# Kernel tuning notes

Hardware: AMD Instinct MI355X
Metric: run time of the kernel (lower is better)

## Reference

```python
import jax, jax.numpy as jnp
import numpy as np

B, S, D, H = 1, 256, 128, 4
HD = D // H          # 32
EPS = 1e-5
SCALE = 1.0 / float(np.sqrt(HD))


def setup_inputs() -> dict:
    key = jax.random.key(0)
    ks = jax.random.split(key, 6)
    pair = jax.random.normal(ks[0], (B, S, S, D), dtype=jnp.float32)
    ln_w = jnp.ones((D,), dtype=jnp.float32)
    wq = jax.random.normal(ks[1], (D, D), dtype=jnp.float32) * 0.05
    wk = jax.random.normal(ks[2], (D, D), dtype=jnp.float32) * 0.05
    wv = jax.random.normal(ks[3], (D, D), dtype=jnp.float32) * 0.05
    wo = jax.random.normal(ks[4], (D, D), dtype=jnp.float32) * 0.05
    return {"pair": pair, "ln_w": ln_w, "wq": wq, "wk": wk, "wv": wv, "wo": wo}


def reference(pair, ln_w, wq, wk, wv, wo):
    b, s, _, d = pair.shape
    h, hd = H, HD
    # LayerNorm (weight only, no bias) over last dim
    mu = jnp.mean(pair, axis=-1, keepdims=True)
    var = jnp.mean((pair - mu) ** 2, axis=-1, keepdims=True)
    xn = (pair - mu) * jax.lax.rsqrt(var + EPS) * ln_w
    # starting=True: no transpose of the pair axes
    q = (xn @ wq.T).reshape(b, s, s, h, hd)
    k = (xn @ wk.T).reshape(b, s, s, h, hd)
    v = (xn @ wv.T).reshape(b, s, s, h, hd)
    # attention over the second seq axis (j), independent per row i
    scores = jnp.einsum("biqhd,bikhd->bihqk", q, k) * SCALE  # [b,i,h,q,k]
    p = jax.nn.softmax(scores, axis=-1)
    out = jnp.einsum("bihqk,bikhd->biqhd", p, v).reshape(b, s, s, d)
    return out @ wo.T
```

## Files before the change

kernel.cpp:

```cpp
#include <hip/hip_runtime.h>
#include <hip/hip_bf16.h>
#include <math.h>

#define S 256
#define D 128
#define H 4
#define HD 32
#define NT (S * S)

constexpr float EPS = 1e-5f;
constexpr float EXPC = 0.17677669529663687f * 1.44269504088896f;

typedef short bf16x8 __attribute__((ext_vector_type(8)));
typedef float floatx4 __attribute__((ext_vector_type(4)));

union BfBits { __hip_bfloat16 b; unsigned short u; };
__device__ inline unsigned short f2bf_bits(float f) {
  BfBits t;
  t.b = __float2bfloat16(f);
  return t.u;
}
__device__ inline short f2bf_s(float f) { return (short)f2bf_bits(f); }
__device__ inline float bfbits2f(unsigned short u) {
  union { float f; unsigned int i; } t;
  t.i = ((unsigned int)u) << 16;
  return t.f;
}
__device__ inline void split_bf(float x, unsigned short& hi, unsigned short& lo) {
  hi = f2bf_bits(x);
  lo = f2bf_bits(x - bfbits2f(hi));
}
__device__ inline unsigned int pk2(float a, float b) {
  return (unsigned int)f2bf_bits(a) | ((unsigned int)f2bf_bits(b) << 16);
}

__global__ __launch_bounds__(256) void wsplit_kernel(
    const float* __restrict__ wq, const float* __restrict__ wk,
    const float* __restrict__ wv, const float* __restrict__ wo,
    unsigned short* __restrict__ whi, unsigned short* __restrict__ wlo) {
  int idx = blockIdx.x * 256 + threadIdx.x;
  const float* srcs[4] = {wq, wk, wv, wo};
#pragma unroll
  for (int m = 0; m < 4; m++) {
    unsigned short hi, lo;
    split_bf(srcs[m][idx], hi, lo);
    whi[m * 16384 + idx] = hi;
    wlo[m * 16384 + idx] = lo;
  }
}

#define XS(row, col) ((col) ^ (((row) & 7) << 3))

__global__ __launch_bounds__(512, 2) void fused_tri_kernel(
    const float* __restrict__ pair, const float* __restrict__ ln_w,
    const unsigned short* __restrict__ Whi,
    const unsigned short* __restrict__ Wlo, float* __restrict__ out) {
  __shared__ unsigned short xn[256][D];
  __shared__ unsigned int kvpool[8192];
  unsigned short* Kt = (unsigned short*)kvpool;
  unsigned short* Vt = (unsigned short*)kvpool + 8192;
  unsigned int* Ost = kvpool;

  const int i = blockIdx.x;
  const int w = (int)(threadIdx.x >> 6);
  const int lane = (int)(threadIdx.x & 63);
  const int c16 = lane & 15;
  const int quad = lane >> 4;
  const int h = w >> 1;
  const int half = w & 1;

  {
    float4 w0 = *(const float4*)(ln_w + c16 * 8);
    float4 w1 = *(const float4*)(ln_w + c16 * 8 + 4);
#pragma unroll
    for (int g = 0; g < 8; g++) {
      const int tok = w * 32 + g * 4 + quad;
      const float* src = pair + ((size_t)i * S + tok) * D + c16 * 8;
      float4 x0 = *(const float4*)(src);
      float4 x1 = *(const float4*)(src + 4);
      float s = (x0.x + x0.y) + (x0.z + x0.w) + (x1.x + x1.y) + (x1.z + x1.w);
      s += __shfl_xor(s, 1);
      s += __shfl_xor(s, 2);
      s += __shfl_xor(s, 4);
      s += __shfl_xor(s, 8);
      const float mu = s * (1.0f / D);
      float a[8];
      a[0] = x0.x - mu; a[1] = x0.y - mu; a[2] = x0.z - mu; a[3] = x0.w - mu;
      a[4] = x1.x - mu; a[5] = x1.y - mu; a[6] = x1.z - mu; a[7] = x1.w - mu;
      float vs = 0.f;
#pragma unroll
      for (int r = 0; r < 8; r++) vs = fmaf(a[r], a[r], vs);
      vs += __shfl_xor(vs, 1);
      vs += __shfl_xor(vs, 2);
      vs += __shfl_xor(vs, 4);
      vs += __shfl_xor(vs, 8);
      const float rinv = rsqrtf(vs * (1.0f / D) + EPS);
      const float wv8[8] = {w0.x, w0.y, w0.z, w0.w, w1.x, w1.y, w1.z, w1.w};
      unsigned int u[4];
#pragma unroll
      for (int r = 0; r < 4; r++) {
        unsigned int h0 = f2bf_bits(a[2 * r] * rinv * wv8[2 * r]);
        unsigned int h1 = f2bf_bits(a[2 * r + 1] * rinv * wv8[2 * r + 1]);
        u[r] = h0 | (h1 << 16);
      }
      uint4 st = {u[0], u[1], u[2], u[3]};
      *(uint4*)&xn[tok][XS(tok, c16 * 8)] = st;
    }
  }
  __syncthreads();

  bf16x8 qf[8];
  {
#pragma unroll
    for (int r = 0; r < 2; r++) {
      floatx4 acc[2][4];
#pragma unroll
      for (int mi = 0; mi < 2; mi++)
#pragma unroll
        for (int nt = 0; nt < 4; nt++) acc[mi][nt] = (floatx4){0.f, 0.f, 0.f, 0.f};
#pragma unroll
      for (int ks = 0; ks < 4; ks++) {
        bf16x8 bh[4];
#pragma unroll
        for (int nt = 0; nt < 4; nt++) {
          const int row = half * 128 + r * 64 + nt * 16 + c16;
          bh[nt] = *(const bf16x8*)&xn[row][XS(row, ks * 32 + quad * 8)];
        }
#pragma unroll
        for (int mi = 0; mi < 2; mi++) {
          const int arow = h * 32 + mi * 16 + c16;
          bf16x8 ah = *(const bf16x8*)(Whi + arow * D + ks * 32 + quad * 8);
          bf16x8 al = *(const bf16x8*)(Wlo + arow * D + ks * 32 + quad * 8);
#pragma unroll
          for (int nt = 0; nt < 4; nt++) {
            acc[mi][nt] = __builtin_amdgcn_mfma_f32_16x16x32_bf16(ah, bh[nt], acc[mi][nt], 0, 0, 0);
            acc[mi][nt] = __builtin_amdgcn_mfma_f32_16x16x32_bf16(al, bh[nt], acc[mi][nt], 0, 0, 0);
          }
        }
      }
      const int srcL = c16 + (quad & 1) * 32;
      const int srcH = srcL + 16;
      const bool hi2 = quad >= 2;
#pragma unroll
      for (int nt = 0; nt < 4; nt++) {
        int pa = (int)pk2(acc[0][nt][0], acc[0][nt][1]);
        int pb = (int)pk2(acc[0][nt][2], acc[0][nt][3]);
        int pc = (int)pk2(acc[1][nt][0], acc[1][nt][1]);
        int pd = (int)pk2(acc[1][nt][2], acc[1][nt][3]);
        int aL = __shfl(pa, srcL), cL = __shfl(pc, srcL);
        int bL = __shfl(pb, srcL), dL = __shfl(pd, srcL);
        int aH = __shfl(pa, srcH), cH = __shfl(pc, srcH);
        int bH = __shfl(pb, srcH), dH = __shfl(pd, srcH);
        union { unsigned int u[4]; bf16x8 v; } qq;
        qq.u[0] = (unsigned int)(hi2 ? cL : aL);
        qq.u[1] = (unsigned int)(hi2 ? dL : bL);
        qq.u[2] = (unsigned int)(hi2 ? cH : aH);
        qq.u[3] = (unsigned int)(hi2 ? dH : bH);
        qf[r * 4 + nt] = qq.v;
      }
    }
  }

  floatx4 att[2][8];
#pragma unroll
  for (int dt = 0; dt < 2; dt++)
#pragma unroll
    for (int qt = 0; qt < 8; qt++) att[dt][qt] = (floatx4){0.f, 0.f, 0.f, 0.f};
  float lsum[8] = {0.f, 0.f, 0.f, 0.f, 0.f, 0.f, 0.f, 0.f};
  const int permc = ((c16 >> 2) * 8) + (c16 & 3);

  for (int jt = 0; jt < 4; jt++) {
    __syncthreads();
    {
      const int hb = half * 16;
      const unsigned short* wkh = Whi + 16384;
      const unsigned short* wkl = Wlo + 16384;
      const unsigned short* wvh = Whi + 32768;
      const unsigned short* wvl = Wlo + 32768;
      floatx4 ak[4], av[4];
#pragma unroll
      for (int nt = 0; nt < 4; nt++) {
        ak[nt] = (floatx4){0.f, 0.f, 0.f, 0.f};
        av[nt] = (floatx4){0.f, 0.f, 0.f, 0.f};
      }
#pragma unroll
      for (int ks = 0; ks < 4; ks++) {
        bf16x8 bh[4];
#pragma unroll
        for (int nt = 0; nt < 4; nt++) {
          const int row = jt * 64 + nt * 16 + c16;
          bh[nt] = *(const bf16x8*)&xn[row][XS(row, ks * 32 + quad * 8)];
        }
        const int arow = h * 32 + hb + c16;
        bf16x8 kh = *(const bf16x8*)(wkh + arow * D + ks * 32 + quad * 8);
        bf16x8 kl = *(const bf16x8*)(wkl + arow * D + ks * 32 + quad * 8);
        bf16x8 vh = *(const bf16x8*)(wvh + arow * D + ks * 32 + quad * 8);
        bf16x8 vl = *(const bf16x8*)(wvl + arow * D + ks * 32 + quad * 8);
#pragma unroll
        for (int nt = 0; nt < 4; nt++) {
          ak[nt] = __builtin_amdgcn_mfma_f32_16x16x32_bf16(kh, bh[nt], ak[nt], 0, 0, 0);
          ak[nt] = __builtin_amdgcn_mfma_f32_16x16x32_bf16(kl, bh[nt], ak[nt], 0, 0, 0);
          av[nt] = __builtin_amdgcn_mfma_f32_16x16x32_bf16(vh, bh[nt], av[nt], 0, 0, 0);
          av[nt] = __builtin_amdgcn_mfma_f32_16x16x32_bf16(vl, bh[nt], av[nt], 0, 0, 0);
        }
      }
      const int c2 = half * 2 + (quad >> 1);
#pragma unroll
      for (int nt = 0; nt < 4; nt++) {
        const int jl = nt * 16 + c16;
        ushort4 pkk;
        pkk.x = f2bf_bits(ak[nt][0]);
        pkk.y = f2bf_bits(ak[nt][1]);
        pkk.z = f2bf_bits(ak[nt][2]);
        pkk.w = f2bf_bits(ak[nt][3]);
        *(ushort4*)(Kt + h * 2048 + c2 * 512 + jl * 8 + (quad & 1) * 4) = pkk;
#pragma unroll
        for (int r2 = 0; r2 < 4; r2++) {
          const int hd = hb + quad * 4 + r2;
          Vt[h * 2048 + hd * 64 + (((jl >> 3) ^ (hd & 7)) << 3) + (jl & 7)] =
              f2bf_bits(av[nt][r2]);
        }
      }
    }
    __syncthreads();
#pragma unroll
    for (int jb = 0; jb < 2; jb++) {
      const int jbl = jb * 32;
      bf16x8 kf0 = *(const bf16x8*)(Kt + h * 2048 + quad * 512 + (jbl + permc) * 8);
      bf16x8 kf1 = *(const bf16x8*)(Kt + h * 2048 + quad * 512 + (jbl + permc + 4) * 8);
      const int ch = (jbl >> 3) + quad;
      bf16x8 vf0 = *(const bf16x8*)(Vt + h * 2048 + c16 * 64 + ((ch ^ (c16 & 7)) << 3));
      bf16x8 vf1 = *(const bf16x8*)(Vt + h * 2048 + (16 + c16) * 64 + ((ch ^ (c16 & 7)) << 3));
#pragma unroll
      for (int qt = 0; qt < 8; qt++) {
        floatx4 s0 = __builtin_amdgcn_mfma_f32_16x16x32_bf16(
            kf0, qf[qt], (floatx4){0.f, 0.f, 0.f, 0.f}, 0, 0, 0);
        floatx4 s1 = __builtin_amdgcn_mfma_f32_16x16x32_bf16(
            kf1, qf[qt], (floatx4){0.f, 0.f, 0.f, 0.f}, 0, 0, 0);
        float pr[8];
#pragma unroll
        for (int r = 0; r < 4; r++) pr[r] = exp2f(s0[r] * EXPC);
#pragma unroll
        for (int r = 0; r < 4; r++) pr[4 + r] = exp2f(s1[r] * EXPC);
        float ls = 0.f;
#pragma unroll
        for (int r = 0; r < 8; r++) ls += pr[r];
        lsum[qt] += ls;
        bf16x8 pf;
#pragma unroll
        for (int r = 0; r < 8; r++) pf[r] = f2bf_s(pr[r]);
        att[0][qt] = __builtin_amdgcn_mfma_f32_16x16x32_bf16(vf0, pf, att[0][qt], 0, 0, 0);
        att[1][qt] = __builtin_amdgcn_mfma_f32_16x16x32_bf16(vf1, pf, att[1][qt], 0, 0, 0);
      }
    }
  }

#pragma unroll
  for (int qt = 0; qt < 8; qt++) {
    float l = lsum[qt];
    l += __shfl_xor(l, 16);
    l += __shfl_xor(l, 32);
    lsum[qt] = 1.0f / l;
  }

  bf16x8 woh[4], wol[4];
#pragma unroll
  for (int ks = 0; ks < 4; ks++) {
    woh[ks] = *(const bf16x8*)(Whi + 3 * 16384 + (w * 16 + c16) * D + ks * 32 + quad * 8);
    wol[ks] = *(const bf16x8*)(Wlo + 3 * 16384 + (w * 16 + c16) * D + ks * 32 + quad * 8);
  }

#pragma unroll
  for (int cc = 0; cc < 4; cc++) {
    __syncthreads();
    if ((cc >> 1) == half) {
#pragma unroll
      for (int t = 0; t < 4; t++) {
        const int qg = (cc & 1) * 4 + t;
        const float inv = lsum[qg];
        const int tok = t * 16 + c16;
#pragma unroll
        for (int dt = 0; dt < 2; dt++) {
          floatx4 v4 = att[dt][qg];
          unsigned int u[4];
          unsigned short hh, ll;
          split_bf(v4[0] * inv, hh, ll); u[0] = (unsigned)hh | ((unsigned)ll << 16);
          split_bf(v4[1] * inv, hh, ll); u[1] = (unsigned)hh | ((unsigned)ll << 16);
          split_bf(v4[2] * inv, hh, ll); u[2] = (unsigned)hh | ((unsigned)ll << 16);
          split_bf(v4[3] * inv, hh, ll); u[3] = (unsigned)hh | ((unsigned)ll << 16);
          const int chunk = h * 8 + dt * 4 + quad;
          uint4 st = {u[0], u[1], u[2], u[3]};
          *(uint4*)(Ost + tok * 128 + ((chunk ^ c16) << 2)) = st;
        }
      }
    }
    __syncthreads();
    floatx4 oacc[4];
#pragma unroll
    for (int nt = 0; nt < 4; nt++) oacc[nt] = (floatx4){0.f, 0.f, 0.f, 0.f};
#pragma unroll
    for (int ks = 0; ks < 4; ks++) {
#pragma unroll
      for (int nt = 0; nt < 4; nt++) {
        const int tok = nt * 16 + c16;
        const int ch0 = ks * 8 + quad * 2;
        uint4 u0 = *(const uint4*)(Ost + tok * 128 + ((ch0 ^ c16) << 2));
        uint4 u1 = *(const uint4*)(Ost + tok * 128 + (((ch0 + 1) ^ c16) << 2));
        unsigned int bhw[4], blw[4];
        bhw[0] = (u0.x & 0xFFFFu) | (u0.y << 16);
        blw[0] = (u0.x >> 16) | (u0.y & 0xFFFF0000u);
        bhw[1] = (u0.z & 0xFFFFu) | (u0.w << 16);
        blw[1] = (u0.z >> 16) | (u0.w & 0xFFFF0000u);
        bhw[2] = (u1.x & 0xFFFFu) | (u1.y << 16);
        blw[2] = (u1.x >> 16) | (u1.y & 0xFFFF0000u);
        bhw[3] = (u1.z & 0xFFFFu) | (u1.w << 16);
        blw[3] = (u1.z >> 16) | (u1.w & 0xFFFF0000u);
        bf16x8 bh = *(bf16x8*)bhw;
        bf16x8 bl = *(bf16x8*)blw;
        oacc[nt] = __builtin_amdgcn_mfma_f32_16x16x32_bf16(woh[ks], bh, oacc[nt], 0, 0, 0);
        oacc[nt] = __builtin_amdgcn_mfma_f32_16x16x32_bf16(woh[ks], bl, oacc[nt], 0, 0, 0);
        oacc[nt] = __builtin_amdgcn_mfma_f32_16x16x32_bf16(wol[ks], bh, oacc[nt], 0, 0, 0);
      }
    }
#pragma unroll
    for (int nt = 0; nt < 4; nt++) {
      float4 st4;
      st4.x = oacc[nt][0];
      st4.y = oacc[nt][1];
      st4.z = oacc[nt][2];
      st4.w = oacc[nt][3];
      *(float4*)(out + ((size_t)i * S + cc * 64 + nt * 16 + c16) * D + w * 16 + quad * 4) = st4;
    }
  }
}

extern "C" void kernel_launch(void* const* d_in, const int* in_sizes, int n_in,
                              void* d_out, int out_size, void* d_ws,
                              size_t ws_size, hipStream_t stream) {
  const float* pair = (const float*)d_in[0];
  const float* ln_w = (const float*)d_in[1];
  const float* wq = (const float*)d_in[2];
  const float* wk = (const float*)d_in[3];
  const float* wv = (const float*)d_in[4];
  const float* wo = (const float*)d_in[5];
  float* out = (float*)d_out;

  unsigned short* Whi = (unsigned short*)d_ws;
  unsigned short* Wlo = Whi + 4 * 16384;

  wsplit_kernel<<<64, 256, 0, stream>>>(wq, wk, wv, wo, Whi, Wlo);
  fused_tri_kernel<<<S, 512, 0, stream>>>(pair, ln_w, Whi, Wlo, out);
}
```

Before: 159.5 us.

## Double-buffer K/V tiles to overlap projection with attention, plus load batching

K/V projection for the next 64-token tile is now computed into registers while attention consumes the current tile from a second shared-memory buffer, which removes one barrier per iteration and lets MFMA projection overlap softmax work. Several smaller changes come with it. All pair loads are issued before the LayerNorm math, and the Q weight fragments are hoisted out of the k-loop. The softmax scale is folded into Q before packing to bf16. The output projection is retiled 32x32 per wave and drops the first barrier. The cost is double the shared memory for K/V and more live registers, which could hurt occupancy under launch_bounds(512,2), and prescaling Q changes bf16 rounding slightly.

```diff
diff --git a/kernel.cpp b/kernel.cpp
--- a/kernel.cpp
+++ b/kernel.cpp
@@ -51,15 +51,111 @@
 
 #define XS(row, col) ((col) ^ (((row) & 7) << 3))
 
+__device__ __forceinline__ floatx4 MF(bf16x8 a, bf16x8 b, floatx4 c) {
+  return __builtin_amdgcn_mfma_f32_16x16x32_bf16(a, b, c, 0, 0, 0);
+}
+
+__device__ __forceinline__ void kv_mfma(const unsigned short (*xn)[D],
+                                        const unsigned short* __restrict__ Whi,
+                                        const unsigned short* __restrict__ Wlo,
+                                        int jt, int h, int hb, int c16,
+                                        int quad, floatx4 ak[4], floatx4 av[4]) {
+  const unsigned short* wkh = Whi + 16384;
+  const unsigned short* wkl = Wlo + 16384;
+  const unsigned short* wvh = Whi + 32768;
+  const unsigned short* wvl = Wlo + 32768;
+  const int arow = h * 32 + hb + c16;
+#pragma unroll
+  for (int nt = 0; nt < 4; nt++) {
+    ak[nt] = (floatx4){0.f, 0.f, 0.f, 0.f};
+    av[nt] = (floatx4){0.f, 0.f, 0.f, 0.f};
+  }
+#pragma unroll
+  for (int ks = 0; ks < 4; ks++) {
+    bf16x8 bh[4];
+#pragma unroll
+    for (int nt = 0; nt < 4; nt++) {
+      const int row = jt * 64 + nt * 16 + c16;
+      bh[nt] = *(const bf16x8*)&xn[row][XS(row, ks * 32 + quad * 8)];
+    }
+    bf16x8 kh = *(const bf16x8*)(wkh + arow * D + ks * 32 + quad * 8);
+    bf16x8 kl = *(const bf16x8*)(wkl + arow * D + ks * 32 + quad * 8);
+    bf16x8 vh = *(const bf16x8*)(wvh + arow * D + ks * 32 + quad * 8);
+    bf16x8 vl = *(const bf16x8*)(wvl + arow * D + ks * 32 + quad * 8);
+#pragma unroll
+    for (int nt = 0; nt < 4; nt++) {
+      ak[nt] = MF(kh, bh[nt], ak[nt]);
+      ak[nt] = MF(kl, bh[nt], ak[nt]);
+      av[nt] = MF(vh, bh[nt], av[nt]);
+      av[nt] = MF(vl, bh[nt], av[nt]);
+    }
+  }
+}
+
+__device__ __forceinline__ void kv_store(unsigned short* Ktb,
+                                         unsigned short* Vtb, int h, int hb,
+                                         int c16, int quad, const floatx4 ak[4],
+                                         const floatx4 av[4]) {
+  const int c2 = (hb >> 3) + (quad >> 1);
+#pragma unroll
+  for (int nt = 0; nt < 4; nt++) {
+    const int jl = nt * 16 + c16;
+    ushort4 pkk;
+    pkk.x = f2bf_bits(ak[nt][0]);
+    pkk.y = f2bf_bits(ak[nt][1]);
+    pkk.z = f2bf_bits(ak[nt][2]);
+    pkk.w = f2bf_bits(ak[nt][3]);
+    *(ushort4*)(Ktb + h * 2048 + c2 * 512 + jl * 8 + (quad & 1) * 4) = pkk;
+#pragma unroll
+    for (int r2 = 0; r2 < 4; r2++) {
+      const int hd = hb + quad * 4 + r2;
+      Vtb[h * 2048 + hd * 64 + (((jl >> 3) ^ (hd & 7)) << 3) + (jl & 7)] =
+          f2bf_bits(av[nt][r2]);
+    }
+  }
+}
+
+__device__ __forceinline__ void attn_consume(const unsigned short* Ktb,
+                                             const unsigned short* Vtb, int h,
+                                             int c16, int quad, int permc,
+                                             const bf16x8 qf[8], floatx4 att0[8],
+                                             floatx4 att1[8], float lsum[8]) {
+#pragma unroll
+  for (int jb = 0; jb < 2; jb++) {
+    const int jbl = jb * 32;
+    bf16x8 kf0 = *(const bf16x8*)(Ktb + h * 2048 + quad * 512 + (jbl + permc) * 8);
+    bf16x8 kf1 = *(const bf16x8*)(Ktb + h * 2048 + quad * 512 + (jbl + permc + 4) * 8);
+    const int ch = (jbl >> 3) + quad;
+    bf16x8 vf0 = *(const bf16x8*)(Vtb + h * 2048 + c16 * 64 + ((ch ^ (c16 & 7)) << 3));
+    bf16x8 vf1 = *(const bf16x8*)(Vtb + h * 2048 + (16 + c16) * 64 + ((ch ^ (c16 & 7)) << 3));
+#pragma unroll
+    for (int qt = 0; qt < 8; qt++) {
+      floatx4 s0 = MF(kf0, qf[qt], (floatx4){0.f, 0.f, 0.f, 0.f});
+      floatx4 s1 = MF(kf1, qf[qt], (floatx4){0.f, 0.f, 0.f, 0.f});
+      float pr[8];
+#pragma unroll
+      for (int r = 0; r < 4; r++) pr[r] = exp2f(s0[r]);
+#pragma unroll
+      for (int r = 0; r < 4; r++) pr[4 + r] = exp2f(s1[r]);
+      float ls = 0.f;
+#pragma unroll
+      for (int r = 0; r < 8; r++) ls += pr[r];
+      lsum[qt] += ls;
+      bf16x8 pf;
+#pragma unroll
+      for (int r = 0; r < 8; r++) pf[r] = f2bf_s(pr[r]);
+      att0[qt] = MF(vf0, pf, att0[qt]);
+      att1[qt] = MF(vf1, pf, att1[qt]);
+    }
+  }
+}
+
 __global__ __launch_bounds__(512, 2) void fused_tri_kernel(
     const float* __restrict__ pair, const float* __restrict__ ln_w,
     const unsigned short* __restrict__ Whi,
     const unsigned short* __restrict__ Wlo, float* __restrict__ out) {
   __shared__ unsigned short xn[256][D];
-  __shared__ unsigned int kvpool[8192];
-  unsigned short* Kt = (unsigned short*)kvpool;
-  unsigned short* Vt = (unsigned short*)kvpool + 8192;
-  unsigned int* Ost = kvpool;
+  __shared__ unsigned int kvpool[2][8192];
 
   const int i = blockIdx.x;
   const int w = (int)(threadIdx.x >> 6);
@@ -68,16 +164,24 @@
   const int quad = lane >> 4;
   const int h = w >> 1;
   const int half = w & 1;
+  const int hb = half * 16;
 
   {
     float4 w0 = *(const float4*)(ln_w + c16 * 8);
     float4 w1 = *(const float4*)(ln_w + c16 * 8 + 4);
+    float4 xr0[8], xr1[8];
 #pragma unroll
     for (int g = 0; g < 8; g++) {
       const int tok = w * 32 + g * 4 + quad;
       const float* src = pair + ((size_t)i * S + tok) * D + c16 * 8;
-      float4 x0 = *(const float4*)(src);
-      float4 x1 = *(const float4*)(src + 4);
+      xr0[g] = *(const float4*)(src);
+      xr1[g] = *(const float4*)(src + 4);
+    }
+#pragma unroll
+    for (int g = 0; g < 8; g++) {
+      const int tok = w * 32 + g * 4 + quad;
+      float4 x0 = xr0[g];
+      float4 x1 = xr1[g];
       float s = (x0.x + x0.y) + (x0.z + x0.w) + (x1.x + x1.y) + (x1.z + x1.w);
       s += __shfl_xor(s, 1);
       s += __shfl_xor(s, 2);
@@ -111,6 +215,15 @@
 
   bf16x8 qf[8];
   {
+    bf16x8 qah[2][4], qal[2][4];
+#pragma unroll
+    for (int mi = 0; mi < 2; mi++)
+#pragma unroll
+      for (int ks = 0; ks < 4; ks++) {
+        const int arow = h * 32 + mi * 16 + c16;
+        qah[mi][ks] = *(const bf16x8*)(Whi + arow * D + ks * 32 + quad * 8);
+        qal[mi][ks] = *(const bf16x8*)(Wlo + arow * D + ks * 32 + quad * 8);
+      }
 #pragma unroll
     for (int r = 0; r < 2; r++) {
       floatx4 acc[2][4];
@@ -127,26 +240,22 @@
           bh[nt] = *(const bf16x8*)&xn[row][XS(row, ks * 32 + quad * 8)];
         }
 #pragma unroll
-        for (int mi = 0; mi < 2; mi++) {
-          const int arow = h * 32 + mi * 16 + c16;
-          bf16x8 ah = *(const bf16x8*)(Whi + arow * D + ks * 32 + quad * 8);
-          bf16x8 al = *(const bf16x8*)(Wlo + arow * D + ks * 32 + quad * 8);
+        for (int mi = 0; mi < 2; mi++)
 #pragma unroll
           for (int nt = 0; nt < 4; nt++) {
-            acc[mi][nt] = __builtin_amdgcn_mfma_f32_16x16x32_bf16(ah, bh[nt], acc[mi][nt], 0, 0, 0);
-            acc[mi][nt] = __builtin_amdgcn_mfma_f32_16x16x32_bf16(al, bh[nt], acc[mi][nt], 0, 0, 0);
+            acc[mi][nt] = MF(qah[mi][ks], bh[nt], acc[mi][nt]);
+            acc[mi][nt] = MF(qal[mi][ks], bh[nt], acc[mi][nt]);
           }
-        }
       }
       const int srcL = c16 + (quad & 1) * 32;
       const int srcH = srcL + 16;
       const bool hi2 = quad >= 2;
 #pragma unroll
       for (int nt = 0; nt < 4; nt++) {
-        int pa = (int)pk2(acc[0][nt][0], acc[0][nt][1]);
-        int pb = (int)pk2(acc[0][nt][2], acc[0][nt][3]);
-        int pc = (int)pk2(acc[1][nt][0], acc[1][nt][1]);
-        int pd = (int)pk2(acc[1][nt][2], acc[1][nt][3]);
+        int pa = (int)pk2(acc[0][nt][0] * EXPC, acc[0][nt][1] * EXPC);
+        int pb = (int)pk2(acc[0][nt][2] * EXPC, acc[0][nt][3] * EXPC);
+        int pc = (int)pk2(acc[1][nt][0] * EXPC, acc[1][nt][1] * EXPC);
+        int pd = (int)pk2(acc[1][nt][2] * EXPC, acc[1][nt][3] * EXPC);
         int aL = __shfl(pa, srcL), cL = __shfl(pc, srcL);
         int bL = __shfl(pb, srcL), dL = __shfl(pd, srcL);
         int aH = __shfl(pa, srcH), cH = __shfl(pc, srcH);
@@ -169,90 +278,21 @@
   float lsum[8] = {0.f, 0.f, 0.f, 0.f, 0.f, 0.f, 0.f, 0.f};
   const int permc = ((c16 >> 2) * 8) + (c16 & 3);
 
+  floatx4 ak[4], av[4];
+  {
+    unsigned short* Kt0 = (unsigned short*)kvpool;
+    kv_mfma(xn, Whi, Wlo, 0, h, hb, c16, quad, ak, av);
+    kv_store(Kt0, Kt0 + 8192, h, hb, c16, quad, ak, av);
+  }
+  __syncthreads();
+
   for (int jt = 0; jt < 4; jt++) {
+    unsigned short* Ktn = (unsigned short*)kvpool + ((jt + 1) & 1) * 16384;
+    const unsigned short* Ktc = (const unsigned short*)kvpool + (jt & 1) * 16384;
+    if (jt < 3) kv_mfma(xn, Whi, Wlo, jt + 1, h, hb, c16, quad, ak, av);
+    attn_consume(Ktc, Ktc + 8192, h, c16, quad, permc, qf, att[0], att[1], lsum);
+    if (jt < 3) kv_store(Ktn, Ktn + 8192, h, hb, c16, quad, ak, av);
     __syncthreads();
-    {
-      const int hb = half * 16;
-      const unsigned short* wkh = Whi + 16384;
-      const unsigned short* wkl = Wlo + 16384;
-      const unsigned short* wvh = Whi + 32768;
-      const unsigned short* wvl = Wlo + 32768;
-      floatx4 ak[4], av[4];
-#pragma unroll
-      for (int nt = 0; nt < 4; nt++) {
-        ak[nt] = (floatx4){0.f, 0.f, 0.f, 0.f};
-        av[nt] = (floatx4){0.f, 0.f, 0.f, 0.f};
-      }
-#pragma unroll
-      for (int ks = 0; ks < 4; ks++) {
-        bf16x8 bh[4];
-#pragma unroll
-        for (int nt = 0; nt < 4; nt++) {
-          const int row = jt * 64 + nt * 16 + c16;
-          bh[nt] = *(const bf16x8*)&xn[row][XS(row, ks * 32 + quad * 8)];
-        }
-        const int arow = h * 32 + hb + c16;
-        bf16x8 kh = *(const bf16x8*)(wkh + arow * D + ks * 32 + quad * 8);
-        bf16x8 kl = *(const bf16x8*)(wkl + arow * D + ks * 32 + quad * 8);
-        bf16x8 vh = *(const bf16x8*)(wvh + arow * D + ks * 32 + quad * 8);
-        bf16x8 vl = *(const bf16x8*)(wvl + arow * D + ks * 32 + quad * 8);
-#pragma unroll
-        for (int nt = 0; nt < 4; nt++) {
-          ak[nt] = __builtin_amdgcn_mfma_f32_16x16x32_bf16(kh, bh[nt], ak[nt], 0, 0, 0);
-          ak[nt] = __builtin_amdgcn_mfma_f32_16x16x32_bf16(kl, bh[nt], ak[nt], 0, 0, 0);
-          av[nt] = __builtin_amdgcn_mfma_f32_16x16x32_bf16(vh, bh[nt], av[nt], 0, 0, 0);
-          av[nt] = __builtin_amdgcn_mfma_f32_16x16x32_bf16(vl, bh[nt], av[nt], 0, 0, 0);
-        }
-      }
-      const int c2 = half * 2 + (quad >> 1);
-#pragma unroll
-      for (int nt = 0; nt < 4; nt++) {
-        const int jl = nt * 16 + c16;
-        ushort4 pkk;
-        pkk.x = f2bf_bits(ak[nt][0]);
-        pkk.y = f2bf_bits(ak[nt][1]);
-        pkk.z = f2bf_bits(ak[nt][2]);
-        pkk.w = f2bf_bits(ak[nt][3]);
-        *(ushort4*)(Kt + h * 2048 + c2 * 512 + jl * 8 + (quad & 1) * 4) = pkk;
-#pragma unroll
-        for (int r2 = 0; r2 < 4; r2++) {
-          const int hd = hb + quad * 4 + r2;
-          Vt[h * 2048 + hd * 64 + (((jl >> 3) ^ (hd & 7)) << 3) + (jl & 7)] =
-              f2bf_bits(av[nt][r2]);
-        }
-      }
-    }
-    __syncthreads();
-#pragma unroll
-    for (int jb = 0; jb < 2; jb++) {
-      const int jbl = jb * 32;
-      bf16x8 kf0 = *(const bf16x8*)(Kt + h * 2048 + quad * 512 + (jbl + permc) * 8);
-      bf16x8 kf1 = *(const bf16x8*)(Kt + h * 2048 + quad * 512 + (jbl + permc + 4) * 8);
-      const int ch = (jbl >> 3) + quad;
-      bf16x8 vf0 = *(const bf16x8*)(Vt + h * 2048 + c16 * 64 + ((ch ^ (c16 & 7)) << 3));
-      bf16x8 vf1 = *(const bf16x8*)(Vt + h * 2048 + (16 + c16) * 64 + ((ch ^ (c16 & 7)) << 3));
-#pragma unroll
-      for (int qt = 0; qt < 8; qt++) {
-        floatx4 s0 = __builtin_amdgcn_mfma_f32_16x16x32_bf16(
-            kf0, qf[qt], (floatx4){0.f, 0.f, 0.f, 0.f}, 0, 0, 0);
-        floatx4 s1 = __builtin_amdgcn_mfma_f32_16x16x32_bf16(
-            kf1, qf[qt], (floatx4){0.f, 0.f, 0.f, 0.f}, 0, 0, 0);
-        float pr[8];
-#pragma unroll
-        for (int r = 0; r < 4; r++) pr[r] = exp2f(s0[r] * EXPC);
-#pragma unroll
-        for (int r = 0; r < 4; r++) pr[4 + r] = exp2f(s1[r] * EXPC);
-        float ls = 0.f;
-#pragma unroll
-        for (int r = 0; r < 8; r++) ls += pr[r];
-        lsum[qt] += ls;
-        bf16x8 pf;
-#pragma unroll
-        for (int r = 0; r < 8; r++) pf[r] = f2bf_s(pr[r]);
-        att[0][qt] = __builtin_amdgcn_mfma_f32_16x16x32_bf16(vf0, pf, att[0][qt], 0, 0, 0);
-        att[1][qt] = __builtin_amdgcn_mfma_f32_16x16x32_bf16(vf1, pf, att[1][qt], 0, 0, 0);
-      }
-    }
   }
 
 #pragma unroll
@@ -263,16 +303,22 @@
     lsum[qt] = 1.0f / l;
   }
 
-  bf16x8 woh[4], wol[4];
-#pragma unroll
-  for (int ks = 0; ks < 4; ks++) {
-    woh[ks] = *(const bf16x8*)(Whi + 3 * 16384 + (w * 16 + c16) * D + ks * 32 + quad * 8);
-    wol[ks] = *(const bf16x8*)(Wlo + 3 * 16384 + (w * 16 + c16) * D + ks * 32 + quad * 8);
-  }
+  const int g32 = w & 3;
+  const int th = w >> 2;
+  bf16x8 woh[2][4], wol[2][4];
+#pragma unroll
+  for (int mi = 0; mi < 2; mi++)
+#pragma unroll
+    for (int ks = 0; ks < 4; ks++) {
+      const int m0 = g32 * 32 + mi * 16;
+      woh[mi][ks] = *(const bf16x8*)(Whi + 3 * 16384 + (m0 + c16) * D + ks * 32 + quad * 8);
+      wol[mi][ks] = *(const bf16x8*)(Wlo + 3 * 16384 + (m0 + c16) * D + ks * 32 + quad * 8);
+    }
+  unsigned int* Ost = (unsigned int*)kvpool;
 
 #pragma unroll
   for (int cc = 0; cc < 4; cc++) {
-    __syncthreads();
+    if (cc) __syncthreads();
     if ((cc >> 1) == half) {
 #pragma unroll
       for (int t = 0; t < 4; t++) {
@@ -295,14 +341,16 @@
       }
     }
     __syncthreads();
-    floatx4 oacc[4];
-#pragma unroll
-    for (int nt = 0; nt < 4; nt++) oacc[nt] = (floatx4){0.f, 0.f, 0.f, 0.f};
+    floatx4 oacc[2][2];
+#pragma unroll
+    for (int mi = 0; mi < 2; mi++)
+#pragma unroll
+      for (int nt2 = 0; nt2 < 2; nt2++) oacc[mi][nt2] = (floatx4){0.f, 0.f, 0.f, 0.f};
 #pragma unroll
     for (int ks = 0; ks < 4; ks++) {
 #pragma unroll
-      for (int nt = 0; nt < 4; nt++) {
-        const int tok = nt * 16 + c16;
+      for (int nt2 = 0; nt2 < 2; nt2++) {
+        const int tok = (th * 2 + nt2) * 16 + c16;
         const int ch0 = ks * 8 + quad * 2;
         uint4 u0 = *(const uint4*)(Ost + tok * 128 + ((ch0 ^ c16) << 2));
         uint4 u1 = *(const uint4*)(Ost + tok * 128 + (((ch0 + 1) ^ c16) << 2));
@@ -317,19 +365,26 @@
         blw[3] = (u1.z >> 16) | (u1.w & 0xFFFF0000u);
         bf16x8 bh = *(bf16x8*)bhw;
         bf16x8 bl = *(bf16x8*)blw;
-        oacc[nt] = __builtin_amdgcn_mfma_f32_16x16x32_bf16(woh[ks], bh, oacc[nt], 0, 0, 0);
-        oacc[nt] = __builtin_amdgcn_mfma_f32_16x16x32_bf16(woh[ks], bl, oacc[nt], 0, 0, 0);
-        oacc[nt] = __builtin_amdgcn_mfma_f32_16x16x32_bf16(wol[ks], bh, oacc[nt], 0, 0, 0);
-      }
-    }
-#pragma unroll
-    for (int nt = 0; nt < 4; nt++) {
-      float4 st4;
-      st4.x = oacc[nt][0];
-      st4.y = oacc[nt][1];
-      st4.z = oacc[nt][2];
-      st4.w = oacc[nt][3];
-      *(float4*)(out + ((size_t)i * S + cc * 64 + nt * 16 + c16) * D + w * 16 + quad * 4) = st4;
+#pragma unroll
+        for (int mi = 0; mi < 2; mi++) {
+          oacc[mi][nt2] = MF(woh[mi][ks], bh, oacc[mi][nt2]);
+          oacc[mi][nt2] = MF(woh[mi][ks], bl, oacc[mi][nt2]);
+          oacc[mi][nt2] = MF(wol[mi][ks], bh, oacc[mi][nt2]);
+        }
+      }
+    }
+#pragma unroll
+    for (int nt2 = 0; nt2 < 2; nt2++) {
+      const int tok = cc * 64 + (th * 2 + nt2) * 16 + c16;
+#pragma unroll
+      for (int mi = 0; mi < 2; mi++) {
+        float4 st4;
+        st4.x = oacc[mi][nt2][0];
+        st4.y = oacc[mi][nt2][1];
+        st4.z = oacc[mi][nt2][2];
+        st4.w = oacc[mi][nt2][3];
+        *(float4*)(out + ((size_t)i * S + tok) * D + g32 * 32 + mi * 16 + quad * 4) = st4;
+      }
     }
   }
 }
```

New measurement: 176.9 us. 10.9% more time.

## Double-buffer K/V tiles and move to 1024-thread blocks with wider work split

Applied to the files above, without the earlier changes.

Block size goes from 512 to 1024 threads, so each of the 16 waves owns fewer query tiles, and the per-row work is redistributed across them. K/V projection for the next 64-token tile is computed into a second shared buffer while the current one is consumed, which removes one barrier per iteration and lets the projection overlap the attention compute. The softmax scale is folded into Q before the exp, and the output projection runs once over the full Ost buffer instead of in four synchronized chunks. In exchange, shared memory use grows to 128KB per block, which limits blocks per CU, and the launch-bounds hint of 4 blocks per CU may constrain registers.

```diff
diff --git a/kernel.cpp b/kernel.cpp
--- a/kernel.cpp
+++ b/kernel.cpp
@@ -6,7 +6,6 @@
 #define D 128
 #define H 4
 #define HD 32
-#define NT (S * S)
 
 constexpr float EPS = 1e-5f;
 constexpr float EXPC = 0.17677669529663687f * 1.44269504088896f;
@@ -51,33 +50,131 @@
 
 #define XS(row, col) ((col) ^ (((row) & 7) << 3))
 
-__global__ __launch_bounds__(512, 2) void fused_tri_kernel(
+__device__ __forceinline__ floatx4 MF(bf16x8 a, bf16x8 b, floatx4 c) {
+  return __builtin_amdgcn_mfma_f32_16x16x32_bf16(a, b, c, 0, 0, 0);
+}
+
+__device__ __forceinline__ void kv_produce(
+    const unsigned short* xn, const unsigned short* __restrict__ Whi,
+    const unsigned short* __restrict__ Wlo, unsigned short* base, int jt,
+    int h, int hb, int jh, int c16, int quad) {
+  unsigned short* Kt = base;
+  unsigned short* Vt = base + 8192;
+  const unsigned short* wkh = Whi + 16384;
+  const unsigned short* wkl = Wlo + 16384;
+  const unsigned short* wvh = Whi + 32768;
+  const unsigned short* wvl = Wlo + 32768;
+  const int arow = h * 32 + hb + c16;
+  floatx4 ak[2], av[2];
+#pragma unroll
+  for (int nt = 0; nt < 2; nt++) {
+    ak[nt] = (floatx4){0.f, 0.f, 0.f, 0.f};
+    av[nt] = (floatx4){0.f, 0.f, 0.f, 0.f};
+  }
+#pragma unroll
+  for (int ks = 0; ks < 4; ks++) {
+    bf16x8 bh[2];
+#pragma unroll
+    for (int nt = 0; nt < 2; nt++) {
+      const int row = jt * 64 + jh * 32 + nt * 16 + c16;
+      bh[nt] = *(const bf16x8*)&xn[row * D + XS(row, ks * 32 + quad * 8)];
+    }
+    bf16x8 kh = *(const bf16x8*)(wkh + arow * D + ks * 32 + quad * 8);
+    bf16x8 kl = *(const bf16x8*)(wkl + arow * D + ks * 32 + quad * 8);
+    bf16x8 vh = *(const bf16x8*)(wvh + arow * D + ks * 32 + quad * 8);
+    bf16x8 vl = *(const bf16x8*)(wvl + arow * D + ks * 32 + quad * 8);
+#pragma unroll
+    for (int nt = 0; nt < 2; nt++) {
+      ak[nt] = MF(kh, bh[nt], ak[nt]);
+      ak[nt] = MF(kl, bh[nt], ak[nt]);
+      av[nt] = MF(vh, bh[nt], av[nt]);
+      av[nt] = MF(vl, bh[nt], av[nt]);
+    }
+  }
+  const int c2 = (hb >> 3) + (quad >> 1);
+#pragma unroll
+  for (int nt = 0; nt < 2; nt++) {
+    const int jl = jh * 32 + nt * 16 + c16;
+    ushort4 pkk;
+    pkk.x = f2bf_bits(ak[nt][0]);
+    pkk.y = f2bf_bits(ak[nt][1]);
+    pkk.z = f2bf_bits(ak[nt][2]);
+    pkk.w = f2bf_bits(ak[nt][3]);
+    *(ushort4*)(Kt + h * 2048 + c2 * 512 + jl * 8 + (quad & 1) * 4) = pkk;
+#pragma unroll
+    for (int r2 = 0; r2 < 4; r2++) {
+      const int hd = hb + quad * 4 + r2;
+      Vt[h * 2048 + hd * 64 + (((jl >> 3) ^ (hd & 7)) << 3) + (jl & 7)] =
+          f2bf_bits(av[nt][r2]);
+    }
+  }
+}
+
+__device__ __forceinline__ void attn_consume(const unsigned short* base, int h,
+                                             int c16, int quad, int permc,
+                                             const bf16x8 qf[4], floatx4 att0[4],
+                                             floatx4 att1[4], float lsum[4]) {
+  const unsigned short* Kt = base;
+  const unsigned short* Vt = base + 8192;
+#pragma unroll
+  for (int jb = 0; jb < 2; jb++) {
+    const int jbl = jb * 32;
+    bf16x8 kf0 = *(const bf16x8*)(Kt + h * 2048 + quad * 512 + (jbl + permc) * 8);
+    bf16x8 kf1 = *(const bf16x8*)(Kt + h * 2048 + quad * 512 + (jbl + permc + 4) * 8);
+    const int ch = (jbl >> 3) + quad;
+    bf16x8 vf0 = *(const bf16x8*)(Vt + h * 2048 + c16 * 64 + ((ch ^ (c16 & 7)) << 3));
+    bf16x8 vf1 = *(const bf16x8*)(Vt + h * 2048 + (16 + c16) * 64 + ((ch ^ (c16 & 7)) << 3));
+#pragma unroll
+    for (int qt = 0; qt < 4; qt++) {
+      floatx4 s0 = MF(kf0, qf[qt], (floatx4){0.f, 0.f, 0.f, 0.f});
+      floatx4 s1 = MF(kf1, qf[qt], (floatx4){0.f, 0.f, 0.f, 0.f});
+      float pr[8];
+#pragma unroll
+      for (int r = 0; r < 4; r++) pr[r] = exp2f(s0[r]);
+#pragma unroll
+      for (int r = 0; r < 4; r++) pr[4 + r] = exp2f(s1[r]);
+      float ls = 0.f;
+#pragma unroll
+      for (int r = 0; r < 8; r++) ls += pr[r];
+      lsum[qt] += ls;
+      bf16x8 pf;
+#pragma unroll
+      for (int r = 0; r < 8; r++) pf[r] = f2bf_s(pr[r]);
+      att0[qt] = MF(vf0, pf, att0[qt]);
+      att1[qt] = MF(vf1, pf, att1[qt]);
+    }
+  }
+}
+
+__global__ __launch_bounds__(1024, 4) void fused_tri_kernel(
     const float* __restrict__ pair, const float* __restrict__ ln_w,
     const unsigned short* __restrict__ Whi,
     const unsigned short* __restrict__ Wlo, float* __restrict__ out) {
-  __shared__ unsigned short xn[256][D];
-  __shared__ unsigned int kvpool[8192];
-  unsigned short* Kt = (unsigned short*)kvpool;
-  unsigned short* Vt = (unsigned short*)kvpool + 8192;
-  unsigned int* Ost = kvpool;
+  __shared__ unsigned int smem[32768];
+  unsigned short* xn = (unsigned short*)smem;
 
   const int i = blockIdx.x;
   const int w = (int)(threadIdx.x >> 6);
   const int lane = (int)(threadIdx.x & 63);
   const int c16 = lane & 15;
   const int quad = lane >> 4;
-  const int h = w >> 1;
-  const int half = w & 1;
 
   {
     float4 w0 = *(const float4*)(ln_w + c16 * 8);
     float4 w1 = *(const float4*)(ln_w + c16 * 8 + 4);
-#pragma unroll
-    for (int g = 0; g < 8; g++) {
-      const int tok = w * 32 + g * 4 + quad;
+    float4 xr0[4], xr1[4];
+#pragma unroll
+    for (int g = 0; g < 4; g++) {
+      const int tok = w * 16 + g * 4 + quad;
       const float* src = pair + ((size_t)i * S + tok) * D + c16 * 8;
-      float4 x0 = *(const float4*)(src);
-      float4 x1 = *(const float4*)(src + 4);
+      xr0[g] = *(const float4*)(src);
+      xr1[g] = *(const float4*)(src + 4);
+    }
+#pragma unroll
+    for (int g = 0; g < 4; g++) {
+      const int tok = w * 16 + g * 4 + quad;
+      float4 x0 = xr0[g];
+      float4 x1 = xr1[g];
       float s = (x0.x + x0.y) + (x0.z + x0.w) + (x1.x + x1.y) + (x1.z + x1.w);
       s += __shfl_xor(s, 1);
       s += __shfl_xor(s, 2);
@@ -104,232 +201,166 @@
         u[r] = h0 | (h1 << 16);
       }
       uint4 st = {u[0], u[1], u[2], u[3]};
-      *(uint4*)&xn[tok][XS(tok, c16 * 8)] = st;
+      *(uint4*)&xn[tok * D + XS(tok, c16 * 8)] = st;
     }
   }
   __syncthreads();
 
-  bf16x8 qf[8];
+  const int h = w >> 2;
+  const int qq = w & 3;
+
+  bf16x8 qf[4];
   {
-#pragma unroll
-    for (int r = 0; r < 2; r++) {
-      floatx4 acc[2][4];
-#pragma unroll
-      for (int mi = 0; mi < 2; mi++)
-#pragma unroll
-        for (int nt = 0; nt < 4; nt++) acc[mi][nt] = (floatx4){0.f, 0.f, 0.f, 0.f};
-#pragma unroll
-      for (int ks = 0; ks < 4; ks++) {
-        bf16x8 bh[4];
+    floatx4 acc[2][4];
+#pragma unroll
+    for (int mi = 0; mi < 2; mi++)
+#pragma unroll
+      for (int nt = 0; nt < 4; nt++) acc[mi][nt] = (floatx4){0.f, 0.f, 0.f, 0.f};
+#pragma unroll
+    for (int ks = 0; ks < 4; ks++) {
+      bf16x8 bh[4];
+#pragma unroll
+      for (int nt = 0; nt < 4; nt++) {
+        const int row = qq * 64 + nt * 16 + c16;
+        bh[nt] = *(const bf16x8*)&xn[row * D + XS(row, ks * 32 + quad * 8)];
+      }
+#pragma unroll
+      for (int mi = 0; mi < 2; mi++) {
+        const int arow = h * 32 + mi * 16 + c16;
+        bf16x8 ah = *(const bf16x8*)(Whi + arow * D + ks * 32 + quad * 8);
+        bf16x8 al = *(const bf16x8*)(Wlo + arow * D + ks * 32 + quad * 8);
 #pragma unroll
         for (int nt = 0; nt < 4; nt++) {
-          const int row = half * 128 + r * 64 + nt * 16 + c16;
-          bh[nt] = *(const bf16x8*)&xn[row][XS(row, ks * 32 + quad * 8)];
-        }
-#pragma unroll
-        for (int mi = 0; mi < 2; mi++) {
-          const int arow = h * 32 + mi * 16 + c16;
-          bf16x8 ah = *(const bf16x8*)(Whi + arow * D + ks * 32 + quad * 8);
-          bf16x8 al = *(const bf16x8*)(Wlo + arow * D + ks * 32 + quad * 8);
-#pragma unroll
-          for (int nt = 0; nt < 4; nt++) {
-            acc[mi][nt] = __builtin_amdgcn_mfma_f32_16x16x32_bf16(ah, bh[nt], acc[mi][nt], 0, 0, 0);
-            acc[mi][nt] = __builtin_amdgcn_mfma_f32_16x16x32_bf16(al, bh[nt], acc[mi][nt], 0, 0, 0);
-          }
+          acc[mi][nt] = MF(ah, bh[nt], acc[mi][nt]);
+          acc[mi][nt] = MF(al, bh[nt], acc[mi][nt]);
         }
       }
-      const int srcL = c16 + (quad & 1) * 32;
-      const int srcH = srcL + 16;
-      const bool hi2 = quad >= 2;
-#pragma unroll
-      for (int nt = 0; nt < 4; nt++) {
-        int pa = (int)pk2(acc[0][nt][0], acc[0][nt][1]);
-        int pb = (int)pk2(acc[0][nt][2], acc[0][nt][3]);
-        int pc = (int)pk2(acc[1][nt][0], acc[1][nt][1]);
-        int pd = (int)pk2(acc[1][nt][2], acc[1][nt][3]);
-        int aL = __shfl(pa, srcL), cL = __shfl(pc, srcL);
-        int bL = __shfl(pb, srcL), dL = __shfl(pd, srcL);
-        int aH = __shfl(pa, srcH), cH = __shfl(pc, srcH);
-        int bH = __shfl(pb, srcH), dH = __shfl(pd, srcH);
-        union { unsigned int u[4]; bf16x8 v; } qq;
-        qq.u[0] = (unsigned int)(hi2 ? cL : aL);
-        qq.u[1] = (unsigned int)(hi2 ? dL : bL);
-        qq.u[2] = (unsigned int)(hi2 ? cH : aH);
-        qq.u[3] = (unsigned int)(hi2 ? dH : bH);
-        qf[r * 4 + nt] = qq.v;
-      }
-    }
-  }
-
-  floatx4 att[2][8];
+    }
+    const int srcL = c16 + (quad & 1) * 32;
+    const int srcH = srcL + 16;
+    const bool hi2 = quad >= 2;
+#pragma unroll
+    for (int nt = 0; nt < 4; nt++) {
+      int pa = (int)pk2(acc[0][nt][0] * EXPC, acc[0][nt][1] * EXPC);
+      int pb = (int)pk2(acc[0][nt][2] * EXPC, acc[0][nt][3] * EXPC);
+      int pc = (int)pk2(acc[1][nt][0] * EXPC, acc[1][nt][1] * EXPC);
+      int pd = (int)pk2(acc[1][nt][2] * EXPC, acc[1][nt][3] * EXPC);
+      int aL = __shfl(pa, srcL), cL = __shfl(pc, srcL);
+      int bL = __shfl(pb, srcL), dL = __shfl(pd, srcL);
+      int aH = __shfl(pa, srcH), cH = __shfl(pc, srcH);
+      int bH = __shfl(pb, srcH), dH = __shfl(pd, srcH);
+      union { unsigned int u[4]; bf16x8 v; } qq_;
+      qq_.u[0] = (unsigned int)(hi2 ? cL : aL);
+      qq_.u[1] = (unsigned int)(hi2 ? dL : bL);
+      qq_.u[2] = (unsigned int)(hi2 ? cH : aH);
+      qq_.u[3] = (unsigned int)(hi2 ? dH : bH);
+      qf[nt] = qq_.v;
+    }
+  }
+
+  floatx4 att[2][4];
 #pragma unroll
   for (int dt = 0; dt < 2; dt++)
 #pragma unroll
-    for (int qt = 0; qt < 8; qt++) att[dt][qt] = (floatx4){0.f, 0.f, 0.f, 0.f};
-  float lsum[8] = {0.f, 0.f, 0.f, 0.f, 0.f, 0.f, 0.f, 0.f};
+    for (int qt = 0; qt < 4; qt++) att[dt][qt] = (floatx4){0.f, 0.f, 0.f, 0.f};
+  float lsum[4] = {0.f, 0.f, 0.f, 0.f};
   const int permc = ((c16 >> 2) * 8) + (c16 & 3);
-
+  const int hb = ((w >> 1) & 1) * 16;
+  const int jh = w & 1;
+
+  unsigned short* kvb = (unsigned short*)(smem + 16384);
+  kv_produce(xn, Whi, Wlo, kvb, 0, h, hb, jh, c16, quad);
+  __syncthreads();
   for (int jt = 0; jt < 4; jt++) {
+    if (jt < 3)
+      kv_produce(xn, Whi, Wlo, kvb + ((jt + 1) & 1) * 16384, jt + 1, h, hb, jh,
+                 c16, quad);
+    attn_consume(kvb + (jt & 1) * 16384, h, c16, quad, permc, qf, att[0],
+                 att[1], lsum);
     __syncthreads();
-    {
-      const int hb = half * 16;
-      const unsigned short* wkh = Whi + 16384;
-      const unsigned short* wkl = Wlo + 16384;
-      const unsigned short* wvh = Whi + 32768;
-      const unsigned short* wvl = Wlo + 32768;
-      floatx4 ak[4], av[4];
-#pragma unroll
-      for (int nt = 0; nt < 4; nt++) {
-        ak[nt] = (floatx4){0.f, 0.f, 0.f, 0.f};
-        av[nt] = (floatx4){0.f, 0.f, 0.f, 0.f};
-      }
-#pragma unroll
-      for (int ks = 0; ks < 4; ks++) {
-        bf16x8 bh[4];
-#pragma unroll
-        for (int nt = 0; nt < 4; nt++) {
-          const int row = jt * 64 + nt * 16 + c16;
-          bh[nt] = *(const bf16x8*)&xn[row][XS(row, ks * 32 + quad * 8)];
-        }
-        const int arow = h * 32 + hb + c16;
-        bf16x8 kh = *(const bf16x8*)(wkh + arow * D + ks * 32 + quad * 8);
-        bf16x8 kl = *(const bf16x8*)(wkl + arow * D + ks * 32 + quad * 8);
-        bf16x8 vh = *(const bf16x8*)(wvh + arow * D + ks * 32 + quad * 8);
-        bf16x8 vl = *(const bf16x8*)(wvl + arow * D + ks * 32 + quad * 8);
-#pragma unroll
-        for (int nt = 0; nt < 4; nt++) {
-          ak[nt] = __builtin_amdgcn_mfma_f32_16x16x32_bf16(kh, bh[nt], ak[nt], 0, 0, 0);
-          ak[nt] = __builtin_amdgcn_mfma_f32_16x16x32_bf16(kl, bh[nt], ak[nt], 0, 0, 0);
-          av[nt] = __builtin_amdgcn_mfma_f32_16x16x32_bf16(vh, bh[nt], av[nt], 0, 0, 0);
-          av[nt] = __builtin_amdgcn_mfma_f32_16x16x32_bf16(vl, bh[nt], av[nt], 0, 0, 0);
-        }
-      }
-      const int c2 = half * 2 + (quad >> 1);
-#pragma unroll
-      for (int nt = 0; nt < 4; nt++) {
-        const int jl = nt * 16 + c16;
-        ushort4 pkk;
-        pkk.x = f2bf_bits(ak[nt][0]);
-        pkk.y = f2bf_bits(ak[nt][1]);
-        pkk.z = f2bf_bits(ak[nt][2]);
-        pkk.w = f2bf_bits(ak[nt][3]);
-        *(ushort4*)(Kt + h * 2048 + c2 * 512 + jl * 8 + (quad & 1) * 4) = pkk;
-#pragma unroll
-        for (int r2 = 0; r2 < 4; r2++) {
-          const int hd = hb + quad * 4 + r2;
-          Vt[h * 2048 + hd * 64 + (((jl >> 3) ^ (hd & 7)) << 3) + (jl & 7)] =
-              f2bf_bits(av[nt][r2]);
-        }
-      }
-    }
-    __syncthreads();
-#pragma unroll
-    for (int jb = 0; jb < 2; jb++) {
-      const int jbl = jb * 32;
-      bf16x8 kf0 = *(const bf16x8*)(Kt + h * 2048 + quad * 512 + (jbl + permc) * 8);
-      bf16x8 kf1 = *(const bf16x8*)(Kt + h * 2048 + quad * 512 + (jbl + permc + 4) * 8);
-      const int ch = (jbl >> 3) + quad;
-      bf16x8 vf0 = *(const bf16x8*)(Vt + h * 2048 + c16 * 64 + ((ch ^ (c16 & 7)) << 3));
-      bf16x8 vf1 = *(const bf16x8*)(Vt + h * 2048 + (16 + c16) * 64 + ((ch ^ (c16 & 7)) << 3));
-#pragma unroll
-      for (int qt = 0; qt < 8; qt++) {
-        floatx4 s0 = __builtin_amdgcn_mfma_f32_16x16x32_bf16(
-            kf0, qf[qt], (floatx4){0.f, 0.f, 0.f, 0.f}, 0, 0, 0);
-        floatx4 s1 = __builtin_amdgcn_mfma_f32_16x16x32_bf16(
-            kf1, qf[qt], (floatx4){0.f, 0.f, 0.f, 0.f}, 0, 0, 0);
-        float pr[8];
-#pragma unroll
-        for (int r = 0; r < 4; r++) pr[r] = exp2f(s0[r] * EXPC);
-#pragma unroll
-        for (int r = 0; r < 4; r++) pr[4 + r] = exp2f(s1[r] * EXPC);
-        float ls = 0.f;
-#pragma unroll
-        for (int r = 0; r < 8; r++) ls += pr[r];
-        lsum[qt] += ls;
-        bf16x8 pf;
-#pragma unroll
-        for (int r = 0; r < 8; r++) pf[r] = f2bf_s(pr[r]);
-        att[0][qt] = __builtin_amdgcn_mfma_f32_16x16x32_bf16(vf0, pf, att[0][qt], 0, 0, 0);
-        att[1][qt] = __builtin_amdgcn_mfma_f32_16x16x32_bf16(vf1, pf, att[1][qt], 0, 0, 0);
-      }
-    }
-  }
-
-#pragma unroll
-  for (int qt = 0; qt < 8; qt++) {
+  }
+
+#pragma unroll
+  for (int qt = 0; qt < 4; qt++) {
     float l = lsum[qt];
     l += __shfl_xor(l, 16);
     l += __shfl_xor(l, 32);
     lsum[qt] = 1.0f / l;
   }
 
-  bf16x8 woh[4], wol[4];
+  unsigned int* Ost = smem;
+#pragma unroll
+  for (int t = 0; t < 4; t++) {
+    const float inv = lsum[t];
+    const int tokg = qq * 64 + t * 16 + c16;
+#pragma unroll
+    for (int dt = 0; dt < 2; dt++) {
+      floatx4 v4 = att[dt][t];
+      unsigned int u[4];
+      unsigned short hh, ll;
+      split_bf(v4[0] * inv, hh, ll); u[0] = (unsigned)hh | ((unsigned)ll << 16);
+      split_bf(v4[1] * inv, hh, ll); u[1] = (unsigned)hh | ((unsigned)ll << 16);
+      split_bf(v4[2] * inv, hh, ll); u[2] = (unsigned)hh | ((unsigned)ll << 16);
+      split_bf(v4[3] * inv, hh, ll); u[3] = (unsigned)hh | ((unsigned)ll << 16);
+      const int chunk = h * 8 + dt * 4 + quad;
+      uint4 st = {u[0], u[1], u[2], u[3]};
+      *(uint4*)(Ost + tokg * 128 + ((chunk ^ c16) << 2)) = st;
+    }
+  }
+  __syncthreads();
+
+  const int g32 = w & 3;
+  const int tq = w >> 2;
+  floatx4 oacc[2][4];
+#pragma unroll
+  for (int mi = 0; mi < 2; mi++)
+#pragma unroll
+    for (int nt = 0; nt < 4; nt++) oacc[mi][nt] = (floatx4){0.f, 0.f, 0.f, 0.f};
 #pragma unroll
   for (int ks = 0; ks < 4; ks++) {
-    woh[ks] = *(const bf16x8*)(Whi + 3 * 16384 + (w * 16 + c16) * D + ks * 32 + quad * 8);
-    wol[ks] = *(const bf16x8*)(Wlo + 3 * 16384 + (w * 16 + c16) * D + ks * 32 + quad * 8);
-  }
-
-#pragma unroll
-  for (int cc = 0; cc < 4; cc++) {
-    __syncthreads();
-    if ((cc >> 1) == half) {
-#pragma unroll
-      for (int t = 0; t < 4; t++) {
-        const int qg = (cc & 1) * 4 + t;
-        const float inv = lsum[qg];
-        const int tok = t * 16 + c16;
-#pragma unroll
-        for (int dt = 0; dt < 2; dt++) {
-          floatx4 v4 = att[dt][qg];
-          unsigned int u[4];
-          unsigned short hh, ll;
-          split_bf(v4[0] * inv, hh, ll); u[0] = (unsigned)hh | ((unsigned)ll << 16);
-          split_bf(v4[1] * inv, hh, ll); u[1] = (unsigned)hh | ((unsigned)ll << 16);
-          split_bf(v4[2] * inv, hh, ll); u[2] = (unsigned)hh | ((unsigned)ll << 16);
-          split_bf(v4[3] * inv, hh, ll); u[3] = (unsigned)hh | ((unsigned)ll << 16);
-          const int chunk = h * 8 + dt * 4 + quad;
-          uint4 st = {u[0], u[1], u[2], u[3]};
-          *(uint4*)(Ost + tok * 128 + ((chunk ^ c16) << 2)) = st;
-        }
+    bf16x8 wo_h[2], wo_l[2];
+#pragma unroll
+    for (int mi = 0; mi < 2; mi++) {
+      const int m0 = g32 * 32 + mi * 16;
+      wo_h[mi] = *(const bf16x8*)(Whi + 3 * 16384 + (m0 + c16) * D + ks * 32 + quad * 8);
+      wo_l[mi] = *(const bf16x8*)(Wlo + 3 * 16384 + (m0 + c16) * D + ks * 32 + quad * 8);
+    }
+#pragma unroll
+    for (int nt = 0; nt < 4; nt++) {
+      const int tok = tq * 64 + nt * 16 + c16;
+      const int ch0 = ks * 8 + quad * 2;
+      uint4 u0 = *(const uint4*)(Ost + tok * 128 + ((ch0 ^ c16) << 2));
+      uint4 u1 = *(const uint4*)(Ost + tok * 128 + (((ch0 + 1) ^ c16) << 2));
+      unsigned int bhw[4], blw[4];
+      bhw[0] = (u0.x & 0xFFFFu) | (u0.y << 16);
+      blw[0] = (u0.x >> 16) | (u0.y & 0xFFFF0000u);
+      bhw[1] = (u0.z & 0xFFFFu) | (u0.w << 16);
+      blw[1] = (u0.z >> 16) | (u0.w & 0xFFFF0000u);
+      bhw[2] = (u1.x & 0xFFFFu) | (u1.y << 16);
+      blw[2] = (u1.x >> 16) | (u1.y & 0xFFFF0000u);
+      bhw[3] = (u1.z & 0xFFFFu) | (u1.w << 16);
+      blw[3] = (u1.z >> 16) | (u1.w & 0xFFFF0000u);
+      bf16x8 bh = *(bf16x8*)bhw;
+      bf16x8 bl = *(bf16x8*)blw;
+#pragma unroll
+      for (int mi = 0; mi < 2; mi++) {
+        oacc[mi][nt] = MF(wo_h[mi], bh, oacc[mi][nt]);
+        oacc[mi][nt] = MF(wo_h[mi], bl, oacc[mi][nt]);
+        oacc[mi][nt] = MF(wo_l[mi], bh, oacc[mi][nt]);
       }
     }
-    __syncthreads();
-    floatx4 oacc[4];
-#pragma unroll
-    for (int nt = 0; nt < 4; nt++) oacc[nt] = (floatx4){0.f, 0.f, 0.f, 0.f};
-#pragma unroll
-    for (int ks = 0; ks < 4; ks++) {
-#pragma unroll
-      for (int nt = 0; nt < 4; nt++) {
-        const int tok = nt * 16 + c16;
-        const int ch0 = ks * 8 + quad * 2;
-        uint4 u0 = *(const uint4*)(Ost + tok * 128 + ((ch0 ^ c16) << 2));
-        uint4 u1 = *(const uint4*)(Ost + tok * 128 + (((ch0 + 1) ^ c16) << 2));
-        unsigned int bhw[4], blw[4];
-        bhw[0] = (u0.x & 0xFFFFu) | (u0.y << 16);
-        blw[0] = (u0.x >> 16) | (u0.y & 0xFFFF0000u);
-        bhw[1] = (u0.z & 0xFFFFu) | (u0.w << 16);
-        blw[1] = (u0.z >> 16) | (u0.w & 0xFFFF0000u);
-        bhw[2] = (u1.x & 0xFFFFu) | (u1.y << 16);
-        blw[2] = (u1.x >> 16) | (u1.y & 0xFFFF0000u);
-        bhw[3] = (u1.z & 0xFFFFu) | (u1.w << 16);
-        blw[3] = (u1.z >> 16) | (u1.w & 0xFFFF0000u);
-        bf16x8 bh = *(bf16x8*)bhw;
-        bf16x8 bl = *(bf16x8*)blw;
-        oacc[nt] = __builtin_amdgcn_mfma_f32_16x16x32_bf16(woh[ks], bh, oacc[nt], 0, 0, 0);
-        oacc[nt] = __builtin_amdgcn_mfma_f32_16x16x32_bf16(woh[ks], bl, oacc[nt], 0, 0, 0);
-        oacc[nt] = __builtin_amdgcn_mfma_f32_16x16x32_bf16(wol[ks], bh, oacc[nt], 0, 0, 0);
-      }
-    }
-#pragma unroll
-    for (int nt = 0; nt < 4; nt++) {
+  }
+#pragma unroll
+  for (int nt = 0; nt < 4; nt++) {
+    const int tok = tq * 64 + nt * 16 + c16;
+#pragma unroll
+    for (int mi = 0; mi < 2; mi++) {
       float4 st4;
-      st4.x = oacc[nt][0];
-      st4.y = oacc[nt][1];
-      st4.z = oacc[nt][2];
-      st4.w = oacc[nt][3];
-      *(float4*)(out + ((size_t)i * S + cc * 64 + nt * 16 + c16) * D + w * 16 + quad * 4) = st4;
+      st4.x = oacc[mi][nt][0];
+      st4.y = oacc[mi][nt][1];
+      st4.z = oacc[mi][nt][2];
+      st4.w = oacc[mi][nt][3];
+      *(float4*)(out + ((size_t)i * S + tok) * D + g32 * 32 + mi * 16 + quad * 4) = st4;
     }
   }
 }
@@ -349,5 +380,5 @@
   unsigned short* Wlo = Whi + 4 * 16384;
 
   wsplit_kernel<<<64, 256, 0, stream>>>(wq, wk, wv, wo, Whi, Wlo);
-  fused_tri_kernel<<<S, 512, 0, stream>>>(pair, ln_w, Whi, Wlo, out);
-}
+  fused_tri_kernel<<<S, 1024, 0, stream>>>(pair, ln_w, Whi, Wlo, out);
+}
```

Result: slower. 188.2 us (+18.0%).
